# Kernel optimization log

Measured on AMD Instinct MI355X. Metric: run time of the kernel, lower is better.

The kernel has to match this reference:

```python
import jax, jax.numpy as jnp
import numpy as np
import math

CHANNELS = 512
N_HEADS = 8
K_CH = CHANNELS // N_HEADS            # 64 per-head dim
ROPE_D = int(K_CH * 0.5)              # 32 dims get RoPE, rest pass through
BASE = 10000


def _rope(x):
    # x: [b, h, t, dk]; rotate first ROPE_D dims (half-split style, matching the torch module)
    d = ROPE_D
    t = x.shape[2]
    theta = 1.0 / (BASE ** (jnp.arange(0, d, 2, dtype=jnp.float32) / d))      # [d/2]
    ang = jnp.arange(t, dtype=jnp.float32)[:, None] * theta[None, :]          # [t, d/2]
    ang = jnp.concatenate([ang, ang], axis=-1)                                # [t, d]
    cos = jnp.cos(ang)[None, None, :, :].astype(x.dtype)
    sin = jnp.sin(ang)[None, None, :, :].astype(x.dtype)
    x_rope, x_pass = x[..., :d], x[..., d:]
    neg_half = jnp.concatenate([-x_rope[..., d // 2:], x_rope[..., :d // 2]], axis=-1)
    return jnp.concatenate([x_rope * cos + neg_half * sin, x_pass], axis=-1)


def _split_heads(y):
    # [b, (h c), t] -> [b, h, t, c]
    b, _, t = y.shape
    return y.reshape(b, N_HEADS, K_CH, t).transpose(0, 1, 3, 2)


def setup_inputs() -> dict:
    key = jax.random.key(0)
    ks = jax.random.split(key, 10)
    B, T = 8, 1024
    w_scale = 1.0 / math.sqrt(CHANNELS)
    return {
        "x": jax.random.normal(ks[0], (B, CHANNELS, T), jnp.float32),
        "c": jax.random.normal(ks[1], (B, CHANNELS, T), jnp.float32),
        "Wq": jax.random.normal(ks[2], (CHANNELS, CHANNELS), jnp.float32) * w_scale,
        "bq": jax.random.normal(ks[3], (CHANNELS,), jnp.float32) * 0.02,
        "Wk": jax.random.normal(ks[4], (CHANNELS, CHANNELS), jnp.float32) * w_scale,
        "bk": jax.random.normal(ks[5], (CHANNELS,), jnp.float32) * 0.02,
        "Wv": jax.random.normal(ks[6], (CHANNELS, CHANNELS), jnp.float32) * w_scale,
        "bv": jax.random.normal(ks[7], (CHANNELS,), jnp.float32) * 0.02,
        "Wo": jax.random.normal(ks[8], (CHANNELS, CHANNELS), jnp.float32) * w_scale,
        "bo": jax.random.normal(ks[9], (CHANNELS,), jnp.float32) * 0.02,
    }


def reference(x, c, Wq, bq, Wk, bk, Wv, bv, Wo, bo):
    # 1x1 Conv1d == per-timestep linear over channels
    q = jnp.einsum('oc,bct->bot', Wq, x) + bq[None, :, None]
    k = jnp.einsum('oc,bct->bot', Wk, c) + bk[None, :, None]
    v = jnp.einsum('oc,bct->bot', Wv, c) + bv[None, :, None]

    q = _rope(_split_heads(q))            # [b,h,t,ck]
    k = _rope(_split_heads(k))            # [b,h,s,ck]
    v = _split_heads(v)                   # [b,h,s,ck]

    scale = 1.0 / math.sqrt(K_CH)
    scores = jnp.einsum('bhtc,bhsc->bhts', q, k) * scale
    p_attn = jax.nn.softmax(scores, axis=-1)       # dropout p=0 -> identity
    out = jnp.einsum('bhts,bhsc->bhtc', p_attn, v)

    b, _, t, _ = out.shape
    out = out.transpose(0, 1, 3, 2).reshape(b, CHANNELS, t)   # [b, (h c), t]
    return jnp.einsum('oc,bct->bot', Wo, out) + bo[None, :, None]
```

## Files before the change

### kernel.cpp

```cpp
#include <hip/hip_runtime.h>

typedef __bf16 bf16x8 __attribute__((ext_vector_type(8)));
typedef float  f32x4  __attribute__((ext_vector_type(4)));

__device__ __forceinline__ unsigned short f2bf(float f){
    union { float f; unsigned u; } v; v.f = f;
    v.u += 0x7fffu + ((v.u >> 16) & 1u);
    return (unsigned short)(v.u >> 16);
}
__device__ __forceinline__ void gl2lds16(const unsigned short* g, unsigned short* l){
    __builtin_amdgcn_global_load_lds(
        (const __attribute__((address_space(1))) void*)g,
        (__attribute__((address_space(3))) void*)l, 16, 0, 0);
}

__global__ __launch_bounds__(256) void transpose_cvt(const float* __restrict__ x, const float* __restrict__ c,
                                                     const float* __restrict__ w0, const float* __restrict__ w1,
                                                     const float* __restrict__ w2, const float* __restrict__ w3,
                                                     unsigned short* __restrict__ xt, unsigned short* __restrict__ ct,
                                                     unsigned short* __restrict__ o0, unsigned short* __restrict__ o1,
                                                     unsigned short* __restrict__ o2, unsigned short* __restrict__ o3){
    __shared__ float tile[64][72];
    const int z = blockIdx.z;
    if (z == 16){
        int fid = (blockIdx.x * 8 + blockIdx.y) * 256 + threadIdx.x;
        const float* in; unsigned short* out;
        switch (fid >> 13){
            case 0: in = w0; out = o0; break;
            case 1: in = w1; out = o1; break;
            case 2: in = w2; out = o2; break;
            default: in = w3; out = o3; break;
        }
        int off = (fid & 8191) * 32;
        #pragma unroll
        for (int j = 0; j < 8; j++){
            float4 v = *(const float4*)(in + off + j*4);
            ushort4 o; o.x = f2bf(v.x); o.y = f2bf(v.y); o.z = f2bf(v.z); o.w = f2bf(v.w);
            *(ushort4*)(out + off + j*4) = o;
        }
        return;
    }
    const float* in = (z < 8) ? x : c;
    unsigned short* out = (z < 8) ? xt : ct;
    const int b = z & 7;
    const int t0 = blockIdx.x * 64, c0 = blockIdx.y * 64;
    const int tid = threadIdx.x;
    {
        int r = tid >> 2, q = (tid & 3) * 16;
        int qs = q ^ (((r >> 4) & 3) << 4);
        const float* src = in + ((size_t)b * 512 + c0 + r) * 1024 + t0 + q;
        #pragma unroll
        for (int j = 0; j < 4; j++)
            *(float4*)&tile[r][qs + j*4] = ((const float4*)src)[j];
    }
    __syncthreads();
    {
        int tr = tid >> 2, cj = (tid & 3) * 16;
        const int fsw = ((cj >> 4) & 3) << 4;
        unsigned pw[8];
        #pragma unroll
        for (int j = 0; j < 8; j++){
            unsigned lo = f2bf(tile[cj + 2*j    ][tr ^ fsw]);
            unsigned hi = f2bf(tile[cj + 2*j + 1][tr ^ fsw]);
            pw[j] = lo | (hi << 16);
        }
        unsigned short* dst = out + ((size_t)b * 1024 + t0 + tr) * 512 + c0 + cj;
        uint4 q0 = {pw[0], pw[1], pw[2], pw[3]};
        uint4 q1 = {pw[4], pw[5], pw[6], pw[7]};
        ((uint4*)dst)[0] = q0;
        ((uint4*)dst)[1] = q1;
    }
}

__device__ __forceinline__ void gemm_mainloop(const unsigned short* __restrict__ A,
                                              const unsigned short* __restrict__ Bm,
                                              unsigned short* a_s, unsigned short* b_s,
                                              int m0, int n0, int tid, f32x4 acc[4][4]){
    const int wave = tid >> 6, lane = tid & 63;
    const int l15 = lane & 15, l4 = lane >> 4;
    const int mw = (wave >> 1) * 64, nw = (wave & 1) * 64;
    const int r8 = lane >> 3, c8l = lane & 7;
    const int csw = (c8l ^ r8) * 8;
    const int rp = l15 & 7;

    auto stage = [&](int k0, int buf){
        unsigned short* as = a_s + buf * (128*64);
        unsigned short* bs = b_s + buf * (128*64);
        #pragma unroll
        for (int i = 0; i < 4; i++){
            int rg = i * 4 + wave;
            int row = rg * 8 + r8;
            gl2lds16(A  + (size_t)(m0 + row) * 512 + k0 + csw, as + rg * 512);
            gl2lds16(Bm + (size_t)(n0 + row) * 512 + k0 + csw, bs + rg * 512);
        }
    };

    stage(0, 0);
    __syncthreads();

    for (int t = 0; t < 8; t++){
        const int buf = t & 1;
        if (t < 7) stage((t + 1) * 64, buf ^ 1);
        const unsigned short* as = a_s + buf * (128*64);
        const unsigned short* bs = b_s + buf * (128*64);
        #pragma unroll
        for (int kk = 0; kk < 2; kk++){
            bf16x8 af[4], bfr[4];
            #pragma unroll
            for (int mt = 0; mt < 4; mt++)
                af[mt] = *(const bf16x8*)&as[(mw + mt*16 + l15)*64 + (((kk*4) + l4) ^ rp)*8];
            #pragma unroll
            for (int ct = 0; ct < 4; ct++)
                bfr[ct] = *(const bf16x8*)&bs[(nw + ct*16 + l15)*64 + (((kk*4) + l4) ^ rp)*8];
            #pragma unroll
            for (int mt = 0; mt < 4; mt++)
                #pragma unroll
                for (int ct = 0; ct < 4; ct++)
                    acc[mt][ct] = __builtin_amdgcn_mfma_f32_16x16x32_bf16(
                        af[mt], bfr[ct], acc[mt][ct], 0, 0, 0);
        }
        __syncthreads();
    }
}

__global__ __launch_bounds__(256) void qkv_gemm(const unsigned short* __restrict__ xt,
                                                const unsigned short* __restrict__ ct,
                                                const unsigned short* __restrict__ wq,
                                                const unsigned short* __restrict__ wk,
                                                const unsigned short* __restrict__ wv,
                                                const float* __restrict__ bq_,
                                                const float* __restrict__ bk_,
                                                const float* __restrict__ bv_,
                                                unsigned short* __restrict__ qt,
                                                unsigned short* __restrict__ kt,
                                                unsigned short* __restrict__ vct){
    __shared__ unsigned short a_s[2*128*64];
    __shared__ unsigned short b_s[2*128*64];
    const int z = blockIdx.y;
    const int xr = blockIdx.x;
    const int bid = (xr & 7) * 32 + (xr >> 3);
    const unsigned short *A, *Bm;
    int m0, n0;
    if (z == 0){ A = xt; Bm = wq; m0 = (bid >> 2)*128; n0 = (bid & 3)*128; }
    else if (z == 1){ A = ct; Bm = wk; m0 = (bid >> 2)*128; n0 = (bid & 3)*128; }
    else { A = wv; Bm = ct; m0 = (bid & 3)*128; n0 = (bid >> 2)*128; }
    const int tid = threadIdx.x;
    const int wave = tid >> 6, lane = tid & 63;
    const int l15 = lane & 15, l4 = lane >> 4;
    const int mw = (wave >> 1) * 64, nw = (wave & 1) * 64;
    const f32x4 vzero = {0.f, 0.f, 0.f, 0.f};
    f32x4 acc[4][4];
    #pragma unroll
    for (int i = 0; i < 4; i++)
        #pragma unroll
        for (int j = 0; j < 4; j++) acc[i][j] = vzero;

    gemm_mainloop(A, Bm, a_s, b_s, m0, n0, tid, acc);

    if (z < 2){
        unsigned short* out = (z == 0) ? qt : kt;
        const float* bias = (z == 0) ? bq_ : bk_;
        const float osc = (z == 0) ? 0.1803368801111137f : 1.0f;
        float bv4[4];
        #pragma unroll
        for (int ct2 = 0; ct2 < 4; ct2++) bv4[ct2] = bias[n0 + nw + ct2*16 + l15];
        const float theta = __powf(10000.0f, -(float)l15 * (1.0f / 16.0f));
        #pragma unroll
        for (int mt = 0; mt < 4; mt++){
            #pragma unroll
            for (int rr = 0; rr < 4; rr++){
                int row = m0 + mw + mt*16 + l4*4 + rr;
                int t = row & 1023;
                float v[4];
                #pragma unroll
                for (int ct2 = 0; ct2 < 4; ct2++) v[ct2] = acc[mt][ct2][rr] + bv4[ct2];
                float sn, cn;
                __sincosf((float)t * theta, &sn, &cn);
                float r0 = v[0] * cn - v[1] * sn;
                float r1 = v[1] * cn + v[0] * sn;
                v[0] = r0; v[1] = r1;
                #pragma unroll
                for (int ct2 = 0; ct2 < 4; ct2++)
                    out[(size_t)row * 512 + n0 + nw + ct2*16 + l15] = f2bf(v[ct2] * osc);
            }
        }
    } else {
        #pragma unroll
        for (int mt = 0; mt < 4; mt++){
            #pragma unroll
            for (int rr = 0; rr < 4; rr++){
                int row = m0 + mw + mt*16 + l4*4 + rr;
                float bb = bv_[row];
                #pragma unroll
                for (int ct2 = 0; ct2 < 4; ct2++){
                    int n = n0 + nw + ct2*16 + l15;
                    size_t oaddr = (size_t)(n >> 10) * 524288 + (size_t)row * 1024 + (n & 1023);
                    vct[oaddr] = f2bf(acc[mt][ct2][rr] + bb);
                }
            }
        }
    }
}

__global__ __launch_bounds__(256) void gemm_o(const unsigned short* __restrict__ wo,
                                              const unsigned short* __restrict__ attnT,
                                              const float* __restrict__ bo,
                                              float* __restrict__ out){
    __shared__ unsigned short a_s[2*64*64];
    __shared__ unsigned short b_s[2*128*64];
    const int m0 = blockIdx.x * 64, n0 = blockIdx.y * 128;
    const int tid = threadIdx.x;
    const int wave = tid >> 6, lane = tid & 63;
    const int l15 = lane & 15, l4 = lane >> 4;
    const int nw = wave * 32;
    const int r8 = lane >> 3, c8l = lane & 7;
    const int csw = (c8l ^ r8) * 8;
    const int rp = l15 & 7;
    const f32x4 vzero = {0.f, 0.f, 0.f, 0.f};
    f32x4 acc[4][2];
    #pragma unroll
    for (int i = 0; i < 4; i++){ acc[i][0] = vzero; acc[i][1] = vzero; }

    auto stage = [&](int k0, int buf){
        unsigned short* as = a_s + buf * (64*64);
        unsigned short* bs = b_s + buf * (128*64);
        #pragma unroll
        for (int i = 0; i < 2; i++){
            int rg = wave * 2 + i;
            gl2lds16(wo + (size_t)(m0 + rg*8 + r8) * 512 + k0 + csw, as + rg * 512);
        }
        #pragma unroll
        for (int i = 0; i < 4; i++){
            int rg = wave * 4 + i;
            gl2lds16(attnT + (size_t)(n0 + rg*8 + r8) * 512 + k0 + csw, bs + rg * 512);
        }
    };

    stage(0, 0);
    __syncthreads();

    for (int t = 0; t < 8; t++){
        const int buf = t & 1;
        if (t < 7) stage((t + 1) * 64, buf ^ 1);
        const unsigned short* as = a_s + buf * (64*64);
        const unsigned short* bs = b_s + buf * (128*64);
        #pragma unroll
        for (int kk = 0; kk < 2; kk++){
            bf16x8 af[4], bfr[2];
            #pragma unroll
            for (int mt = 0; mt < 4; mt++)
                af[mt] = *(const bf16x8*)&as[(mt*16 + l15)*64 + (((kk*4) + l4) ^ rp)*8];
            #pragma unroll
            for (int ct = 0; ct < 2; ct++)
                bfr[ct] = *(const bf16x8*)&bs[(nw + ct*16 + l15)*64 + (((kk*4) + l4) ^ rp)*8];
            #pragma unroll
            for (int mt = 0; mt < 4; mt++)
                #pragma unroll
                for (int ct = 0; ct < 2; ct++)
                    acc[mt][ct] = __builtin_amdgcn_mfma_f32_16x16x32_bf16(
                        af[mt], bfr[ct], acc[mt][ct], 0, 0, 0);
        }
        __syncthreads();
    }

    #pragma unroll
    for (int mt = 0; mt < 4; mt++){
        #pragma unroll
        for (int rr = 0; rr < 4; rr++){
            int row = m0 + mt*16 + l4*4 + rr;
            float bb = bo[row];
            #pragma unroll
            for (int ct2 = 0; ct2 < 2; ct2++){
                int n = n0 + nw + ct2*16 + l15;
                size_t oaddr = (size_t)(n >> 10) * 524288 + (size_t)row * 1024 + (n & 1023);
                out[oaddr] = acc[mt][ct2][rr] + bb;
            }
        }
    }
}

__global__ __launch_bounds__(256, 2) void flash_attn(const unsigned short* __restrict__ qt,
                                                     const unsigned short* __restrict__ kt,
                                                     const unsigned short* __restrict__ vct,
                                                     unsigned short* __restrict__ attnT){
    __shared__ unsigned short k_s[3][64*64];
    __shared__ unsigned short v_s[3][64*64];
    const int bhq = blockIdx.x;
    const int bh = bhq & 63, b = bh >> 3, h = bh & 7;
    const int q0 = (bhq >> 6) * 128;
    const int tid = threadIdx.x, wave = tid >> 6, lane = tid & 63;
    const int l15 = lane & 15, l4 = lane >> 4;
    const int r8 = lane >> 3, c8l = lane & 7;
    const int csw = (c8l ^ r8) * 8;
    const int rp = l15 & 7;
    const f32x4 vzero = {0.f, 0.f, 0.f, 0.f};
    const unsigned short* kbase = kt  + (size_t)(b*1024)*512 + h*64;
    const unsigned short* vbase = vct + (size_t)(b*512 + h*64)*1024;

    bf16x8 qf[2][2];
    #pragma unroll
    for (int st = 0; st < 2; st++)
        #pragma unroll
        for (int kh = 0; kh < 2; kh++)
            qf[st][kh] = *(const bf16x8*)(qt + (size_t)(b*1024 + q0 + wave*32 + st*16 + l15)*512
                                             + h*64 + kh*32 + l4*8);
    f32x4 o_acc[2][4], l_acc[2];
    #pragma unroll
    for (int st = 0; st < 2; st++){
        l_acc[st] = vzero;
        #pragma unroll
        for (int dt = 0; dt < 4; dt++) o_acc[st][dt] = vzero;
    }
    const __bf16 one_bf = (__bf16)1.0f;
    const bf16x8 ones = {one_bf, one_bf, one_bf, one_bf, one_bf, one_bf, one_bf, one_bf};

    auto stage = [&](int tile, int buf){
        const int s0n = tile * 64;
        #pragma unroll
        for (int i = 0; i < 2; i++){
            int rg = i * 4 + wave;
            int row = rg * 8 + r8;
            gl2lds16(kbase + (size_t)(s0n + row)*512 + csw, &k_s[buf][rg*512]);
            gl2lds16(vbase + (size_t)row*1024 + s0n + csw, &v_s[buf][rg*512]);
        }
    };
    stage(0, 0);
    stage(1, 1);

    const int voff0 = (l4 & 1) * 4;
    for (int it = 0; it < 16; ++it){
        const int cur = it % 3;
        if (it == 15) asm volatile("s_waitcnt vmcnt(0)" ::: "memory");
        else          asm volatile("s_waitcnt vmcnt(4)" ::: "memory");
        __builtin_amdgcn_s_barrier();
        if (it < 14) stage(it + 2, (it + 2) % 3);

        bf16x8 kf[2][4];
        #pragma unroll
        for (int kh = 0; kh < 2; kh++)
            #pragma unroll
            for (int ct = 0; ct < 4; ct++)
                kf[kh][ct] = *(const bf16x8*)&k_s[cur][(ct*16 + l15)*64 + ((kh*4 + l4) ^ rp)*8];
        union bfv { bf16x8 v; uint2 u[2]; };
        bfv vfp[2][4];
        #pragma unroll
        for (int c2 = 0; c2 < 2; c2++)
            #pragma unroll
            for (int dt = 0; dt < 4; dt++){
                const int base = (dt*16 + l15)*64;
                const int ch0 = ((c2*4 +     (l4 >> 1)) ^ rp)*8 + voff0;
                const int ch1 = ((c2*4 + 2 + (l4 >> 1)) ^ rp)*8 + voff0;
                vfp[c2][dt].u[0] = *(const uint2*)&v_s[cur][base + ch0];
                vfp[c2][dt].u[1] = *(const uint2*)&v_s[cur][base + ch1];
            }
        #pragma unroll
        for (int st = 0; st < 2; st++){
            f32x4 sa[4];
            #pragma unroll
            for (int ct = 0; ct < 4; ct++) sa[ct] = vzero;
            #pragma unroll
            for (int kh = 0; kh < 2; kh++)
                #pragma unroll
                for (int ct = 0; ct < 4; ct++)
                    sa[ct] = __builtin_amdgcn_mfma_f32_16x16x32_bf16(kf[kh][ct], qf[st][kh], sa[ct], 0, 0, 0);
            #pragma unroll
            for (int ct = 0; ct < 4; ct++)
                #pragma unroll
                for (int rr = 0; rr < 4; rr++)
                    sa[ct][rr] = exp2f(sa[ct][rr]);
            bf16x8 ap[2];
            #pragma unroll
            for (int c2 = 0; c2 < 2; c2++){
                union { unsigned u[4]; bf16x8 v; } pw;
                #pragma unroll
                for (int c1 = 0; c1 < 2; c1++){
                    union { float f; unsigned u; } x0, x1, x2, x3;
                    x0.f = sa[2*c2+c1][0]; x1.f = sa[2*c2+c1][1];
                    x2.f = sa[2*c2+c1][2]; x3.f = sa[2*c2+c1][3];
                    pw.u[c1*2+0] = (x0.u >> 16) | (x1.u & 0xffff0000u);
                    pw.u[c1*2+1] = (x2.u >> 16) | (x3.u & 0xffff0000u);
                }
                ap[c2] = pw.v;
            }
            l_acc[st] = __builtin_amdgcn_mfma_f32_16x16x32_bf16(ap[0], ones, l_acc[st], 0, 0, 0);
            l_acc[st] = __builtin_amdgcn_mfma_f32_16x16x32_bf16(ap[1], ones, l_acc[st], 0, 0, 0);
            #pragma unroll
            for (int dt = 0; dt < 4; dt++){
                o_acc[st][dt] = __builtin_amdgcn_mfma_f32_16x16x32_bf16(ap[0], vfp[0][dt].v, o_acc[st][dt], 0, 0, 0);
                o_acc[st][dt] = __builtin_amdgcn_mfma_f32_16x16x32_bf16(ap[1], vfp[1][dt].v, o_acc[st][dt], 0, 0, 0);
            }
        }
    }
    #pragma unroll
    for (int st = 0; st < 2; st++){
        float rl[4];
        #pragma unroll
        for (int rr = 0; rr < 4; rr++) rl[rr] = __builtin_amdgcn_rcpf(l_acc[st][rr]);
        #pragma unroll
        for (int dt = 0; dt < 4; dt++)
            #pragma unroll
            for (int rr = 0; rr < 4; rr++){
                int row = q0 + wave*32 + st*16 + l4*4 + rr;
                attnT[(size_t)(b*1024 + row)*512 + h*64 + dt*16 + l15] = f2bf(o_acc[st][dt][rr] * rl[rr]);
            }
    }
}

extern "C" void kernel_launch(void* const* d_in, const int* in_sizes, int n_in,
                              void* d_out, int out_size, void* d_ws, size_t ws_size,
                              hipStream_t stream){
    const float* x  = (const float*)d_in[0];
    const float* c  = (const float*)d_in[1];
    const float* Wq = (const float*)d_in[2];
    const float* bq = (const float*)d_in[3];
    const float* Wk = (const float*)d_in[4];
    const float* bk = (const float*)d_in[5];
    const float* Wv = (const float*)d_in[6];
    const float* bv = (const float*)d_in[7];
    const float* Wo = (const float*)d_in[8];
    const float* bo = (const float*)d_in[9];

    unsigned short* wq_b = (unsigned short*)d_ws;
    unsigned short* wk_b = wq_b + 262144;
    unsigned short* wv_b = wk_b + 262144;
    unsigned short* wo_b = wv_b + 262144;
    unsigned short* xt   = wo_b + 262144;
    unsigned short* ct   = xt  + 4194304;
    unsigned short* qt   = ct  + 4194304;
    unsigned short* kt   = qt  + 4194304;
    unsigned short* vct  = kt  + 4194304;
    unsigned short* attnT = xt;

    transpose_cvt<<<dim3(16, 8, 17), 256, 0, stream>>>(x, c, Wq, Wk, Wv, Wo,
                                                       xt, ct, wq_b, wk_b, wv_b, wo_b);
    qkv_gemm<<<dim3(256, 3), 256, 0, stream>>>(xt, ct, wq_b, wk_b, wv_b, bq, bk, bv, qt, kt, vct);
    flash_attn<<<dim3(512), 256, 0, stream>>>(qt, kt, vct, attnT);
    gemm_o<<<dim3(8, 64), 256, 0, stream>>>(wo_b, attnT, bo, (float*)d_out);
}
```

Before: 163.9 us.

## Load QKV GEMM B operand directly from global into registers, raise occupancy

The QKV projection GEMM no longer stages the B operand through LDS; each wave loads its B fragments straight from global memory into registers, which halves the kernel's shared-memory footprint. Launch bounds are raised to 4 blocks per CU for the GEMM and to 3 for flash attention. This aims to cut LDS traffic and barrier cost and to allow more resident blocks. The risk is uncoalesced or redundant global loads of B, since both waves sharing an N half fetch the same data, plus register pressure that could cause spills under the tighter bounds.

```diff
diff --git a/kernel.cpp b/kernel.cpp
--- a/kernel.cpp
+++ b/kernel.cpp
@@ -72,70 +72,18 @@
     }
 }
 
-__device__ __forceinline__ void gemm_mainloop(const unsigned short* __restrict__ A,
-                                              const unsigned short* __restrict__ Bm,
-                                              unsigned short* a_s, unsigned short* b_s,
-                                              int m0, int n0, int tid, f32x4 acc[4][4]){
-    const int wave = tid >> 6, lane = tid & 63;
-    const int l15 = lane & 15, l4 = lane >> 4;
-    const int mw = (wave >> 1) * 64, nw = (wave & 1) * 64;
-    const int r8 = lane >> 3, c8l = lane & 7;
-    const int csw = (c8l ^ r8) * 8;
-    const int rp = l15 & 7;
-
-    auto stage = [&](int k0, int buf){
-        unsigned short* as = a_s + buf * (128*64);
-        unsigned short* bs = b_s + buf * (128*64);
-        #pragma unroll
-        for (int i = 0; i < 4; i++){
-            int rg = i * 4 + wave;
-            int row = rg * 8 + r8;
-            gl2lds16(A  + (size_t)(m0 + row) * 512 + k0 + csw, as + rg * 512);
-            gl2lds16(Bm + (size_t)(n0 + row) * 512 + k0 + csw, bs + rg * 512);
-        }
-    };
-
-    stage(0, 0);
-    __syncthreads();
-
-    for (int t = 0; t < 8; t++){
-        const int buf = t & 1;
-        if (t < 7) stage((t + 1) * 64, buf ^ 1);
-        const unsigned short* as = a_s + buf * (128*64);
-        const unsigned short* bs = b_s + buf * (128*64);
-        #pragma unroll
-        for (int kk = 0; kk < 2; kk++){
-            bf16x8 af[4], bfr[4];
-            #pragma unroll
-            for (int mt = 0; mt < 4; mt++)
-                af[mt] = *(const bf16x8*)&as[(mw + mt*16 + l15)*64 + (((kk*4) + l4) ^ rp)*8];
-            #pragma unroll
-            for (int ct = 0; ct < 4; ct++)
-                bfr[ct] = *(const bf16x8*)&bs[(nw + ct*16 + l15)*64 + (((kk*4) + l4) ^ rp)*8];
-            #pragma unroll
-            for (int mt = 0; mt < 4; mt++)
-                #pragma unroll
-                for (int ct = 0; ct < 4; ct++)
-                    acc[mt][ct] = __builtin_amdgcn_mfma_f32_16x16x32_bf16(
-                        af[mt], bfr[ct], acc[mt][ct], 0, 0, 0);
-        }
-        __syncthreads();
-    }
-}
-
-__global__ __launch_bounds__(256) void qkv_gemm(const unsigned short* __restrict__ xt,
-                                                const unsigned short* __restrict__ ct,
-                                                const unsigned short* __restrict__ wq,
-                                                const unsigned short* __restrict__ wk,
-                                                const unsigned short* __restrict__ wv,
-                                                const float* __restrict__ bq_,
-                                                const float* __restrict__ bk_,
-                                                const float* __restrict__ bv_,
-                                                unsigned short* __restrict__ qt,
-                                                unsigned short* __restrict__ kt,
-                                                unsigned short* __restrict__ vct){
+__global__ __launch_bounds__(256, 4) void qkv_gemm(const unsigned short* __restrict__ xt,
+                                                   const unsigned short* __restrict__ ct,
+                                                   const unsigned short* __restrict__ wq,
+                                                   const unsigned short* __restrict__ wk,
+                                                   const unsigned short* __restrict__ wv,
+                                                   const float* __restrict__ bq_,
+                                                   const float* __restrict__ bk_,
+                                                   const float* __restrict__ bv_,
+                                                   unsigned short* __restrict__ qt,
+                                                   unsigned short* __restrict__ kt,
+                                                   unsigned short* __restrict__ vct){
     __shared__ unsigned short a_s[2*128*64];
-    __shared__ unsigned short b_s[2*128*64];
     const int z = blockIdx.y;
     const int xr = blockIdx.x;
     const int bid = (xr & 7) * 32 + (xr >> 3);
@@ -148,6 +96,9 @@
     const int wave = tid >> 6, lane = tid & 63;
     const int l15 = lane & 15, l4 = lane >> 4;
     const int mw = (wave >> 1) * 64, nw = (wave & 1) * 64;
+    const int r8 = lane >> 3, c8l = lane & 7;
+    const int csw = (c8l ^ r8) * 8;
+    const int rp = l15 & 7;
     const f32x4 vzero = {0.f, 0.f, 0.f, 0.f};
     f32x4 acc[4][4];
     #pragma unroll
@@ -155,7 +106,46 @@
         #pragma unroll
         for (int j = 0; j < 4; j++) acc[i][j] = vzero;
 
-    gemm_mainloop(A, Bm, a_s, b_s, m0, n0, tid, acc);
+    auto stageA = [&](int k0, int buf){
+        unsigned short* as = a_s + buf * (128*64);
+        #pragma unroll
+        for (int i = 0; i < 4; i++){
+            int rg = i * 4 + wave;
+            int row = rg * 8 + r8;
+            gl2lds16(A + (size_t)(m0 + row) * 512 + k0 + csw, as + rg * 512);
+        }
+    };
+    const unsigned short* bbase = Bm + (size_t)(n0 + nw + l15) * 512;
+
+    stageA(0, 0);
+    __syncthreads();
+
+    for (int t = 0; t < 8; t++){
+        const int buf = t & 1;
+        const int k0 = t * 64;
+        if (t < 7) stageA(k0 + 64, buf ^ 1);
+        bf16x8 bfr[2][4];
+        #pragma unroll
+        for (int kk = 0; kk < 2; kk++)
+            #pragma unroll
+            for (int ct2 = 0; ct2 < 4; ct2++)
+                bfr[kk][ct2] = *(const bf16x8*)(bbase + (size_t)(ct2*16)*512 + k0 + kk*32 + l4*8);
+        const unsigned short* as = a_s + buf * (128*64);
+        #pragma unroll
+        for (int kk = 0; kk < 2; kk++){
+            bf16x8 af[4];
+            #pragma unroll
+            for (int mt = 0; mt < 4; mt++)
+                af[mt] = *(const bf16x8*)&as[(mw + mt*16 + l15)*64 + (((kk*4) + l4) ^ rp)*8];
+            #pragma unroll
+            for (int mt = 0; mt < 4; mt++)
+                #pragma unroll
+                for (int ct2 = 0; ct2 < 4; ct2++)
+                    acc[mt][ct2] = __builtin_amdgcn_mfma_f32_16x16x32_bf16(
+                        af[mt], bfr[kk][ct2], acc[mt][ct2], 0, 0, 0);
+        }
+        __syncthreads();
+    }
 
     if (z < 2){
         unsigned short* out = (z == 0) ? qt : kt;
@@ -279,7 +269,7 @@
     }
 }
 
-__global__ __launch_bounds__(256, 2) void flash_attn(const unsigned short* __restrict__ qt,
+__global__ __launch_bounds__(256, 3) void flash_attn(const unsigned short* __restrict__ qt,
                                                      const unsigned short* __restrict__ kt,
                                                      const unsigned short* __restrict__ vct,
                                                      unsigned short* __restrict__ attnT){
```

Result: slower. 177.3 us (+8.1%).
